# Performance work log

Hardware: AMD Instinct MI355X
Metric: run time of the kernel (lower is better)

Reference implementation:

```python
import jax, jax.numpy as jnp
import numpy as np

VOCAB, DIM, LAYERS = 32000, 1024, 4
B, L = 8, 512


def setup_inputs() -> dict:
    key = jax.random.key(0)
    ks = jax.random.split(key, 8)
    s = 0.02
    return {
        "input_ids": jax.random.randint(ks[0], (B, L), 0, VOCAB),
        "embed_W": jax.random.normal(ks[1], (VOCAB, DIM), jnp.float32) * s,
        "h_starter": jax.random.normal(ks[2], (LAYERS, DIM), jnp.float32) * s,
        "gate_W": jax.random.normal(ks[3], (LAYERS, 2 * DIM, 2 * DIM), jnp.float32) * s,
        "gate_b": jnp.zeros((LAYERS, 2 * DIM), jnp.float32),
        "cand_W": jax.random.normal(ks[4], (LAYERS, DIM, 2 * DIM), jnp.float32) * s,
        "cand_b": jnp.zeros((LAYERS, DIM), jnp.float32),
        "out_W": jax.random.normal(ks[5], (VOCAB, DIM), jnp.float32) * s,
    }


def _gru_forward(input_ids, embed_W, h_starter, gate_W, gate_b, cand_W, cand_b, out_W):
    Bsz = input_ids.shape[0]
    x = embed_W[input_ids]                      # [B, L, D]
    h0 = jnp.broadcast_to(h_starter[:, None, :], (LAYERS, Bsz, DIM))  # [Ly, B, D]

    def step(h, x_t):
        # h: [Ly, B, D], x_t: [B, D]
        new_h = []
        xin = x_t
        for i in range(LAYERS):
            hi = h[i]
            xh = jnp.concatenate([xin, hi], axis=-1)           # [B, 2D]
            g = xh @ gate_W[i].T + gate_b[i]                   # [B, 2D]
            z, r = jnp.split(g, 2, axis=-1)
            z = jax.nn.sigmoid(z)
            r = jax.nn.sigmoid(r)
            cin = jnp.concatenate([xin, r * hi], axis=-1)      # [B, 2D]
            cand = jnp.tanh(cin @ cand_W[i].T + cand_b[i])     # [B, D]
            hn = z * hi + (1.0 - z) * cand
            new_h.append(hn)
            xin = hn
        return jnp.stack(new_h), xin

    _, ys = jax.lax.scan(step, h0, jnp.swapaxes(x, 0, 1))      # ys: [L, B, D]
    ys = jnp.swapaxes(ys, 0, 1)                                # [B, L, D]
    logits = jnp.einsum('bld,vd->blv', ys, out_W)              # [B, L, V]
    return logits


def reference(input_ids, embed_W, h_starter, gate_W, gate_b, cand_W, cand_b, out_W):
    return _gru_forward(input_ids, embed_W, h_starter, gate_W, gate_b, cand_W, cand_b, out_W)
```

## Files before the change

### kernel.cpp

```cpp
#include <hip/hip_runtime.h>
#include <hip/hip_bf16.h>

#define VOCAB  32000
#define DIM    1024
#define NLAYER 4
#define NB     8
#define SEQ    512

#define NGROUP       4
#define GBLKS        64
#define SCAN_BLOCKS  (NGROUP * GBLKS)
#define SCAN_THREADS 512
#define ROWH         2056

typedef __attribute__((ext_vector_type(8))) short          bf16x8;
typedef __attribute__((ext_vector_type(4))) float          f32x4;
typedef __attribute__((ext_vector_type(8))) unsigned short u16x8;
typedef __attribute__((ext_vector_type(8))) _Float16       h8f;

__device__ __forceinline__ u16x8 cvt8_bf16(const float* p) {
    float4 f0 = *(const float4*)p;
    float4 f1 = *(const float4*)(p + 4);
    union { __hip_bfloat16 h[8]; u16x8 v; } u;
    u.h[0] = __float2bfloat16(f0.x); u.h[1] = __float2bfloat16(f0.y);
    u.h[2] = __float2bfloat16(f0.z); u.h[3] = __float2bfloat16(f0.w);
    u.h[4] = __float2bfloat16(f1.x); u.h[5] = __float2bfloat16(f1.y);
    u.h[6] = __float2bfloat16(f1.z); u.h[7] = __float2bfloat16(f1.w);
    return u.v;
}

__device__ __forceinline__ h8f pack8(f32x4 a, f32x4 b) {
    h8f o;
    o[0] = (_Float16)a[0]; o[1] = (_Float16)a[1];
    o[2] = (_Float16)a[2]; o[3] = (_Float16)a[3];
    o[4] = (_Float16)b[0]; o[5] = (_Float16)b[1];
    o[6] = (_Float16)b[2]; o[7] = (_Float16)b[3];
    return o;
}

__device__ __forceinline__ void ld4v(f32x4& d, const float* p) {
    asm volatile("global_load_dwordx4 %0, %1, off sc0 sc1"
                 : "=&v"(d) : "v"(p));
}
__device__ __forceinline__ void st1v(float* p, float v) {
    asm volatile("global_store_dword %0, %1, off sc0 sc1"
                 :: "v"(p), "v"(v) : "memory");
}
__device__ __forceinline__ void vmwait0() {
    asm volatile("s_waitcnt vmcnt(0)" ::: "memory");
}

__global__ void bar_init_kernel(unsigned* __restrict__ bar) {
    bar[threadIdx.x]        = 0u;
    bar[threadIdx.x + 1024] = 0u;
    bar[threadIdx.x + 2048] = 0u;
    bar[threadIdx.x + 3072] = 0u;
}

__device__ __forceinline__ void slot_bar(unsigned* __restrict__ slots, int bkg,
                                         unsigned seq, bool& dead) {
    __syncthreads();
    const int tid = threadIdx.x;
    if (tid == 0)
        __hip_atomic_store(&slots[bkg * 8], seq, __ATOMIC_RELAXED,
                           __HIP_MEMORY_SCOPE_AGENT);
    if (tid < 64 && !dead) {
        unsigned guard = 0;
        for (;;) {
            unsigned v = __hip_atomic_load(&slots[tid * 8], __ATOMIC_RELAXED,
                                           __HIP_MEMORY_SCOPE_AGENT);
            if (__all((int)(v >= seq))) break;
            __builtin_amdgcn_s_sleep(1);
            if (++guard > (1u << 16)) { dead = true; break; }
        }
    }
    __syncthreads();
}

__global__ void __launch_bounds__(SCAN_THREADS)
__attribute__((amdgpu_waves_per_eu(2, 2)))
gru_scan(
    const int*   __restrict__ ids,
    const float* __restrict__ embW,
    const float* __restrict__ hstart,
    const float* __restrict__ gW,
    const float* __restrict__ gB,
    const float* __restrict__ cW,
    const float* __restrict__ cB,
    float* __restrict__ hbuf,
    float* __restrict__ rbuf,
    float* __restrict__ ysf,
    unsigned* __restrict__ bar)
{
    __shared__ _Float16 act[NB][ROWH];
    __shared__ float pz[4][4][64];
    __shared__ float pr[4][4][64];
    __shared__ float pc[2][4][64];
    __shared__ float pcb[2][4][64];

    const int tid   = threadIdx.x;
    const int lane  = tid & 63;
    const int wv    = tid >> 6;
    const int l15   = lane & 15;
    const int lgq   = lane >> 4;
    const int bcol  = l15 & 7;
    const int g     = blockIdx.x >> 6;
    const int bkg   = blockIdx.x & (GBLKS-1);
    const int jbase = bkg * 16;
    const int jrow  = jbase + l15;

    h8f Wa[16], Wb[16];
    if (wv < 4) {
        const int kb = wv * 512;
        const float* wzp = gW + ((size_t)g * 2048 + jrow) * 2048;
        const float* wrp = gW + ((size_t)g * 2048 + 1024 + jrow) * 2048;
        #pragma unroll
        for (int kc = 0; kc < 16; ++kc) {
            const int k0 = kb + kc * 32 + lgq * 8;
            Wa[kc] = pack8(*(const f32x4*)(wzp + k0), *(const f32x4*)(wzp + k0 + 4));
            Wb[kc] = pack8(*(const f32x4*)(wrp + k0), *(const f32x4*)(wrp + k0 + 4));
        }
        #pragma unroll
        for (int kc = 0; kc < 16; ++kc) {
            asm volatile("" : "+v"(Wa[kc]));
            asm volatile("" : "+v"(Wb[kc]));
        }
    } else if (wv < 6) {
        const int kb = (wv - 4) * 512;
        const float* wcp = cW + ((size_t)g * 1024 + jrow) * 2048;
        #pragma unroll
        for (int kc = 0; kc < 16; ++kc) {
            const int k0 = kb + kc * 32 + lgq * 8;
            Wa[kc] = pack8(*(const f32x4*)(wcp + k0), *(const f32x4*)(wcp + k0 + 4));
            Wb[kc] = pack8(*(const f32x4*)(wcp + 1024 + k0), *(const f32x4*)(wcp + 1024 + k0 + 4));
        }
        #pragma unroll
        for (int kc = 0; kc < 16; ++kc) {
            asm volatile("" : "+v"(Wa[kc]));
            asm volatile("" : "+v"(Wb[kc]));
        }
    }

    float bz4[4], br4[4], cb4[4], hold[4], zreg[4];
    if (wv == 6) {
        #pragma unroll
        for (int r = 0; r < 4; ++r) {
            const int j = jbase + lgq * 4 + r;
            bz4[r]  = gB[g * 2048 + j];
            cb4[r]  = cB[g * 1024 + j];
            hold[r] = hstart[g * 1024 + j];
        }
    }
    if (wv == 7) {
        #pragma unroll
        for (int r = 0; r < 4; ++r)
            br4[r] = gB[g * 2048 + 1024 + jbase + lgq * 4 + r];
    }

    bool dead = false;
    unsigned* slots1g = bar + g * 512;
    unsigned* slots2g = bar + 2048 + g * 512;
    unsigned* s2prev  = (g > 0)          ? bar + 2048 + (g - 1) * 512 : nullptr;
    unsigned* s1next  = (g < NGROUP - 1) ? bar + (g + 1) * 512        : nullptr;
    float* rbufg = rbuf + (size_t)g * NB * DIM;

    if (tid < 128) {
        int e = bkg * 128 + tid;
        st1v(&hbuf[((size_t)3 * NLAYER + g) * NB * DIM + e],
             hstart[g * DIM + (e & (DIM - 1))]);
    }
    slot_bar(slots2g, bkg, 1u, dead);

    for (int t = 0; t < SEQ; ++t) {
        const int so = (t + 3) & 3;
        const int sw = t & 3;
        const float* hsrc = hbuf + ((size_t)so * NLAYER + g) * NB * DIM;
        float*       hdst = hbuf + ((size_t)sw * NLAYER + g) * NB * DIM;

        {
            const unsigned need_a = (g > 0) ? (unsigned)(t + 2) : 0u;
            const unsigned need_b = (g < NGROUP - 1 && t >= 4) ? (unsigned)(t - 3) : 0u;
            if (tid < 64 && !dead && (need_a | need_b)) {
                unsigned guard = 0;
                for (;;) {
                    bool ok = true;
                    if (need_a)
                        ok &= (__hip_atomic_load(&s2prev[tid * 8], __ATOMIC_RELAXED,
                                                 __HIP_MEMORY_SCOPE_AGENT) >= need_a);
                    if (need_b)
                        ok &= (__hip_atomic_load(&s1next[tid * 8], __ATOMIC_RELAXED,
                                                 __HIP_MEMORY_SCOPE_AGENT) >= need_b);
                    if (__all((int)ok)) break;
                    __builtin_amdgcn_s_sleep(1);
                    if (++guard > (1u << 16)) { dead = true; break; }
                }
            }
            __syncthreads();
        }

        {
            const int ub = tid & 127;
            const int b0 = tid >> 7;
            f32x4 xv0, xv1, xv2, xv3, hv0, hv1, hv2, hv3;
            if (g == 0) {
                const float* s0 = embW + (size_t)ids[b0 * SEQ + t] * DIM + ub * 8;
                const float* s1 = embW + (size_t)ids[(b0 + 4) * SEQ + t] * DIM + ub * 8;
                xv0 = *(const f32x4*)s0; xv1 = *(const f32x4*)(s0 + 4);
                xv2 = *(const f32x4*)s1; xv3 = *(const f32x4*)(s1 + 4);
            } else {
                const float* src = hbuf + ((size_t)sw * NLAYER + (g - 1)) * NB * DIM;
                ld4v(xv0, src + b0 * DIM + ub * 8);
                ld4v(xv1, src + b0 * DIM + ub * 8 + 4);
                ld4v(xv2, src + (b0 + 4) * DIM + ub * 8);
                ld4v(xv3, src + (b0 + 4) * DIM + ub * 8 + 4);
            }
            ld4v(hv0, hsrc + b0 * DIM + ub * 8);
            ld4v(hv1, hsrc + b0 * DIM + ub * 8 + 4);
            ld4v(hv2, hsrc + (b0 + 4) * DIM + ub * 8);
            ld4v(hv3, hsrc + (b0 + 4) * DIM + ub * 8 + 4);
            vmwait0();
            asm volatile("" : "+v"(xv0), "+v"(xv1), "+v"(xv2), "+v"(xv3),
                             "+v"(hv0), "+v"(hv1), "+v"(hv2), "+v"(hv3));
            *(h8f*)&act[b0][ub * 8]            = pack8(xv0, xv1);
            *(h8f*)&act[b0 + 4][ub * 8]        = pack8(xv2, xv3);
            *(h8f*)&act[b0][1024 + ub * 8]     = pack8(hv0, hv1);
            *(h8f*)&act[b0 + 4][1024 + ub * 8] = pack8(hv2, hv3);
        }
        __syncthreads();

        if (wv < 6) {
            const int kb2 = (wv < 4) ? wv * 512 : (wv - 4) * 512;
            f32x4 accA = {0.f, 0.f, 0.f, 0.f};
            f32x4 accB = {0.f, 0.f, 0.f, 0.f};
            #pragma unroll
            for (int kc = 0; kc < 16; ++kc) {
                const h8f bf = *(const h8f*)&act[bcol][kb2 + kc * 32 + lgq * 8];
                accA = __builtin_amdgcn_mfma_f32_16x16x32_f16(Wa[kc], bf, accA, 0, 0, 0);
                if (wv < 4)
                    accB = __builtin_amdgcn_mfma_f32_16x16x32_f16(Wb[kc], bf, accB, 0, 0, 0);
            }
            if (wv < 4) {
                #pragma unroll
                for (int r = 0; r < 4; ++r) {
                    pz[wv][r][lane] = accA[r];
                    pr[wv][r][lane] = accB[r];
                }
            } else {
                #pragma unroll
                for (int r = 0; r < 4; ++r) pc[wv - 4][r][lane] = accA[r];
            }
        }
        __syncthreads();

        if (wv == 6) {
            #pragma unroll
            for (int r = 0; r < 4; ++r) {
                const float s = pz[0][r][lane] + pz[1][r][lane]
                              + pz[2][r][lane] + pz[3][r][lane] + bz4[r];
                zreg[r] = 1.f / (1.f + expf(-s));
            }
        }
        if (wv == 7) {
            #pragma unroll
            for (int r = 0; r < 4; ++r) {
                const float s = pr[0][r][lane] + pr[1][r][lane]
                              + pr[2][r][lane] + pr[3][r][lane] + br4[r];
                const float rg = 1.f / (1.f + expf(-s));
                if (l15 < 8)
                    st1v(rbufg + bcol * DIM + jbase + lgq * 4 + r, rg);
            }
        }
        slot_bar(slots1g, bkg, (unsigned)(t + 1), dead);

        {
            const int ub = tid & 127;
            const int b0 = tid >> 7;
            f32x4 rv0, rv1, rv2, rv3;
            ld4v(rv0, rbufg + b0 * DIM + ub * 8);
            ld4v(rv1, rbufg + b0 * DIM + ub * 8 + 4);
            ld4v(rv2, rbufg + (b0 + 4) * DIM + ub * 8);
            ld4v(rv3, rbufg + (b0 + 4) * DIM + ub * 8 + 4);
            h8f hh0 = *(const h8f*)&act[b0][1024 + ub * 8];
            h8f hh1 = *(const h8f*)&act[b0 + 4][1024 + ub * 8];
            vmwait0();
            asm volatile("" : "+v"(rv0), "+v"(rv1), "+v"(rv2), "+v"(rv3));
            h8f o0, o1;
            #pragma unroll
            for (int i = 0; i < 4; ++i) {
                o0[i]     = (_Float16)((float)hh0[i]     * rv0[i]);
                o0[i + 4] = (_Float16)((float)hh0[i + 4] * rv1[i]);
                o1[i]     = (_Float16)((float)hh1[i]     * rv2[i]);
                o1[i + 4] = (_Float16)((float)hh1[i + 4] * rv3[i]);
            }
            *(h8f*)&act[b0][ub * 8]     = o0;
            *(h8f*)&act[b0 + 4][ub * 8] = o1;
        }
        __syncthreads();

        if (wv == 4 || wv == 5) {
            const int kb2 = (wv - 4) * 512;
            f32x4 acc = {0.f, 0.f, 0.f, 0.f};
            #pragma unroll
            for (int kc = 0; kc < 16; ++kc) {
                const h8f bf = *(const h8f*)&act[bcol][kb2 + kc * 32 + lgq * 8];
                acc = __builtin_amdgcn_mfma_f32_16x16x32_f16(Wb[kc], bf, acc, 0, 0, 0);
            }
            #pragma unroll
            for (int r = 0; r < 4; ++r) pcb[wv - 4][r][lane] = acc[r];
        }
        __syncthreads();

        if (wv == 6) {
            #pragma unroll
            for (int r = 0; r < 4; ++r) {
                const float cand = tanhf(pc[0][r][lane] + pc[1][r][lane]
                                         + pcb[0][r][lane] + pcb[1][r][lane] + cb4[r]);
                const float hn = zreg[r] * hold[r] + (1.f - zreg[r]) * cand;
                hold[r] = hn;
                if (l15 < 8) {
                    const int j = jbase + lgq * 4 + r;
                    st1v(hdst + bcol * DIM + j, hn);
                    if (g == NGROUP - 1)
                        ysf[((size_t)bcol * SEQ + t) * DIM + j] = hn;
                }
            }
        }
        slot_bar(slots2g, bkg, (unsigned)(t + 2), dead);
    }

    if (dead && tid == 0)
        ysf[blockIdx.x] = 1.0e8f;
}

#define BM 128
#define BN 128
#define BK 64

__global__ void __launch_bounds__(256) out_gemm(
    const float* __restrict__ A,
    const float* __restrict__ B,
    float* __restrict__ C)
{
    __shared__ __hip_bfloat16 At[BM][BK + 8];
    __shared__ __hip_bfloat16 Bt[BN][BK + 8];

    const int tid  = threadIdx.x;
    const int lane = tid & 63;
    const int wv   = tid >> 6;
    const int wm   = wv >> 1, wn = wv & 1;
    const int m0   = blockIdx.y * BM;
    const int n0   = blockIdx.x * BN;

    f32x4 acc[4][4];
    #pragma unroll
    for (int i = 0; i < 4; ++i)
        #pragma unroll
        for (int jj = 0; jj < 4; ++jj)
            acc[i][jj] = (f32x4){0.f, 0.f, 0.f, 0.f};

    const int srow = tid >> 3;
    const int scol = (tid & 7) * 8;
    const int l15  = lane & 15;
    const int l4   = lane >> 4;

    for (int kt = 0; kt < DIM / BK; ++kt) {
        const int k0 = kt * BK;
        #pragma unroll
        for (int rnd = 0; rnd < 4; ++rnd) {
            const int row = rnd * 32 + srow;
            *(u16x8*)&At[row][scol] =
                cvt8_bf16(&A[(size_t)(m0 + row) * DIM + k0 + scol]);
            *(u16x8*)&Bt[row][scol] =
                cvt8_bf16(&B[(size_t)(n0 + row) * DIM + k0 + scol]);
        }
        __syncthreads();
        #pragma unroll
        for (int ks = 0; ks < 2; ++ks) {
            bf16x8 av[4], bv[4];
            #pragma unroll
            for (int i = 0; i < 4; ++i) {
                av[i] = *(const bf16x8*)&At[wm * 64 + i * 16 + l15][ks * 32 + l4 * 8];
                bv[i] = *(const bf16x8*)&Bt[wn * 64 + i * 16 + l15][ks * 32 + l4 * 8];
            }
            #pragma unroll
            for (int i = 0; i < 4; ++i)
                #pragma unroll
                for (int jj = 0; jj < 4; ++jj)
                    acc[i][jj] = __builtin_amdgcn_mfma_f32_16x16x32_bf16(
                        av[i], bv[jj], acc[i][jj], 0, 0, 0);
        }
        __syncthreads();
    }

    const int rq = l4 * 4;
    #pragma unroll
    for (int i = 0; i < 4; ++i) {
        const int rbase = m0 + wm * 64 + i * 16 + rq;
        #pragma unroll
        for (int jj = 0; jj < 4; ++jj) {
            const int col = n0 + wn * 64 + jj * 16 + l15;
            #pragma unroll
            for (int r2 = 0; r2 < 4; ++r2)
                C[(size_t)(rbase + r2) * VOCAB + col] = acc[i][jj][r2];
        }
    }
}

extern "C" void kernel_launch(void* const* d_in, const int* in_sizes, int n_in,
                              void* d_out, int out_size, void* d_ws, size_t ws_size,
                              hipStream_t stream)
{
    (void)in_sizes; (void)n_in; (void)out_size; (void)ws_size;
    const int*   ids  = (const int*)  d_in[0];
    const float* embW = (const float*)d_in[1];
    const float* hst  = (const float*)d_in[2];
    const float* gW   = (const float*)d_in[3];
    const float* gB   = (const float*)d_in[4];
    const float* cW   = (const float*)d_in[5];
    const float* cB   = (const float*)d_in[6];
    const float* outW = (const float*)d_in[7];
    float* logits = (float*)d_out;

    char* ws = (char*)d_ws;
    unsigned* bar  = (unsigned*)ws;
    float*    rbuf = (float*)(ws + 16384);
    float*    hbuf = (float*)(ws + 16384 + 131072);
    float*    ysf  = (float*)(ws + 16384 + 131072 + 524288);

    bar_init_kernel<<<dim3(1), dim3(1024), 0, stream>>>(bar);

    gru_scan<<<dim3(SCAN_BLOCKS), dim3(SCAN_THREADS), 0, stream>>>(
        ids, embW, hst, gW, gB, cW, cB, hbuf, rbuf, ysf, bar);

    out_gemm<<<dim3(VOCAB / BN, (NB * SEQ) / BM), dim3(256), 0, stream>>>(ysf, outW, logits);
}
```

Baseline: 4.163 ms.

## Stream fp16 state directly into MFMA operands, drop LDS staging and syncs

The per-step exchange buffers for hidden state and r*h become fp16, and r*h is computed by the gate wave before publishing, so the candidate waves load MFMA B-operands straight from global memory instead of staging everything through a shared activation array. Waits on the previous and next group are moved into only the waves that need them, and two block-wide syncs per step are removed. The final-layer output is written as bf16 so the output GEMM skips its fp32-to-bf16 conversion. In exchange the state exchange loses precision and each wave issues more scattered small global loads.

Result: slower. 6.747 ms (+62.1%).

```diff
diff --git a/kernel.cpp b/kernel.cpp
--- a/kernel.cpp
+++ b/kernel.cpp
@@ -11,12 +11,14 @@
 #define GBLKS        64
 #define SCAN_BLOCKS  (NGROUP * GBLKS)
 #define SCAN_THREADS 512
-#define ROWH         2056
 
 typedef __attribute__((ext_vector_type(8))) short          bf16x8;
 typedef __attribute__((ext_vector_type(4))) float          f32x4;
+typedef __attribute__((ext_vector_type(2))) float          f32x2;
 typedef __attribute__((ext_vector_type(8))) unsigned short u16x8;
+typedef __attribute__((ext_vector_type(4))) unsigned short u16x4;
 typedef __attribute__((ext_vector_type(8))) _Float16       h8f;
+typedef __attribute__((ext_vector_type(4))) _Float16       h4f;
 
 __device__ __forceinline__ u16x8 cvt8_bf16(const float* p) {
     float4 f0 = *(const float4*)p;
@@ -42,8 +44,12 @@
     asm volatile("global_load_dwordx4 %0, %1, off sc0 sc1"
                  : "=&v"(d) : "v"(p));
 }
-__device__ __forceinline__ void st1v(float* p, float v) {
-    asm volatile("global_store_dword %0, %1, off sc0 sc1"
+__device__ __forceinline__ void st8v(void* p, f32x2 v) {
+    asm volatile("global_store_dwordx2 %0, %1, off sc0 sc1"
+                 :: "v"(p), "v"(v) : "memory");
+}
+__device__ __forceinline__ void st2v(void* p, unsigned v) {
+    asm volatile("global_store_short %0, %1, off sc0 sc1"
                  :: "v"(p), "v"(v) : "memory");
 }
 __device__ __forceinline__ void vmwait0() {
@@ -87,16 +93,16 @@
     const float* __restrict__ gB,
     const float* __restrict__ cW,
     const float* __restrict__ cB,
-    float* __restrict__ hbuf,
-    float* __restrict__ rbuf,
-    float* __restrict__ ysf,
+    _Float16* __restrict__ hbuf16,
+    _Float16* __restrict__ rbuf16,
+    __hip_bfloat16* __restrict__ ysfb,
     unsigned* __restrict__ bar)
 {
-    __shared__ _Float16 act[NB][ROWH];
     __shared__ float pz[4][4][64];
     __shared__ float pr[4][4][64];
     __shared__ float pc[2][4][64];
     __shared__ float pcb[2][4][64];
+    __shared__ float hb[4][64];
 
     const int tid   = threadIdx.x;
     const int lane  = tid & 63;
@@ -109,30 +115,30 @@
     const int jbase = bkg * 16;
     const int jrow  = jbase + l15;
 
+    const bool xwave = (wv == 0 || wv == 1 || wv == 4 || wv == 5);
+    const int  xoff  = (wv == 1 || wv == 5) ? 512 : 0;
+    const int  hoff  = (wv == 3) ? 512 : 0;
+
     h8f Wa[16], Wb[16];
-    if (wv < 4) {
-        const int kb = wv * 512;
+    if (wv < 6) {
         const float* wzp = gW + ((size_t)g * 2048 + jrow) * 2048;
         const float* wrp = gW + ((size_t)g * 2048 + 1024 + jrow) * 2048;
+        const float* wcp = cW + ((size_t)g * 1024 + jrow) * 2048;
+        const float* baseA; const float* baseB; int koA, koB;
+        switch (wv) {
+          case 0:  baseA = wzp; koA = 0;    baseB = wrp; koB = 0;    break;
+          case 1:  baseA = wzp; koA = 512;  baseB = wrp; koB = 512;  break;
+          case 2:  baseA = wzp; koA = 1024; baseB = wrp; koB = 1024; break;
+          case 3:  baseA = wzp; koA = 1536; baseB = wrp; koB = 1536; break;
+          case 4:  baseA = wcp; koA = 0;    baseB = wcp; koB = 1024; break;
+          default: baseA = wcp; koA = 512;  baseB = wcp; koB = 1536; break;
+        }
         #pragma unroll
         for (int kc = 0; kc < 16; ++kc) {
-            const int k0 = kb + kc * 32 + lgq * 8;
-            Wa[kc] = pack8(*(const f32x4*)(wzp + k0), *(const f32x4*)(wzp + k0 + 4));
-            Wb[kc] = pack8(*(const f32x4*)(wrp + k0), *(const f32x4*)(wrp + k0 + 4));
-        }
-        #pragma unroll
-        for (int kc = 0; kc < 16; ++kc) {
-            asm volatile("" : "+v"(Wa[kc]));
-            asm volatile("" : "+v"(Wb[kc]));
-        }
-    } else if (wv < 6) {
-        const int kb = (wv - 4) * 512;
-        const float* wcp = cW + ((size_t)g * 1024 + jrow) * 2048;
-        #pragma unroll
-        for (int kc = 0; kc < 16; ++kc) {
-            const int k0 = kb + kc * 32 + lgq * 8;
-            Wa[kc] = pack8(*(const f32x4*)(wcp + k0), *(const f32x4*)(wcp + k0 + 4));
-            Wb[kc] = pack8(*(const f32x4*)(wcp + 1024 + k0), *(const f32x4*)(wcp + 1024 + k0 + 4));
+            const int ka = koA + kc * 32 + lgq * 8;
+            const int kb = koB + kc * 32 + lgq * 8;
+            Wa[kc] = pack8(*(const f32x4*)(baseA + ka), *(const f32x4*)(baseA + ka + 4));
+            Wb[kc] = pack8(*(const f32x4*)(baseB + kb), *(const f32x4*)(baseB + kb + 4));
         }
         #pragma unroll
         for (int kc = 0; kc < 16; ++kc) {
@@ -149,6 +155,7 @@
             bz4[r]  = gB[g * 2048 + j];
             cb4[r]  = cB[g * 1024 + j];
             hold[r] = hstart[g * 1024 + j];
+            hb[r][lane] = hold[r];
         }
     }
     if (wv == 7) {
@@ -162,82 +169,94 @@
     unsigned* slots2g = bar + 2048 + g * 512;
     unsigned* s2prev  = (g > 0)          ? bar + 2048 + (g - 1) * 512 : nullptr;
     unsigned* s1next  = (g < NGROUP - 1) ? bar + (g + 1) * 512        : nullptr;
-    float* rbufg = rbuf + (size_t)g * NB * DIM;
+    _Float16* rbufg16 = rbuf16 + (size_t)g * NB * DIM;
 
     if (tid < 128) {
         int e = bkg * 128 + tid;
-        st1v(&hbuf[((size_t)3 * NLAYER + g) * NB * DIM + e],
-             hstart[g * DIM + (e & (DIM - 1))]);
+        union { _Float16 h; unsigned short u; } cv;
+        cv.h = (_Float16)hstart[g * DIM + (e & (DIM - 1))];
+        st2v(&hbuf16[((size_t)3 * NLAYER + g) * NB * DIM + e], (unsigned)cv.u);
     }
     slot_bar(slots2g, bkg, 1u, dead);
 
     for (int t = 0; t < SEQ; ++t) {
         const int so = (t + 3) & 3;
         const int sw = t & 3;
-        const float* hsrc = hbuf + ((size_t)so * NLAYER + g) * NB * DIM;
-        float*       hdst = hbuf + ((size_t)sw * NLAYER + g) * NB * DIM;
-
-        {
-            const unsigned need_a = (g > 0) ? (unsigned)(t + 2) : 0u;
-            const unsigned need_b = (g < NGROUP - 1 && t >= 4) ? (unsigned)(t - 3) : 0u;
-            if (tid < 64 && !dead && (need_a | need_b)) {
-                unsigned guard = 0;
-                for (;;) {
-                    bool ok = true;
-                    if (need_a)
-                        ok &= (__hip_atomic_load(&s2prev[tid * 8], __ATOMIC_RELAXED,
-                                                 __HIP_MEMORY_SCOPE_AGENT) >= need_a);
-                    if (need_b)
-                        ok &= (__hip_atomic_load(&s1next[tid * 8], __ATOMIC_RELAXED,
-                                                 __HIP_MEMORY_SCOPE_AGENT) >= need_b);
-                    if (__all((int)ok)) break;
-                    __builtin_amdgcn_s_sleep(1);
-                    if (++guard > (1u << 16)) { dead = true; break; }
-                }
-            }
-            __syncthreads();
-        }
-
-        {
-            const int ub = tid & 127;
-            const int b0 = tid >> 7;
-            f32x4 xv0, xv1, xv2, xv3, hv0, hv1, hv2, hv3;
-            if (g == 0) {
-                const float* s0 = embW + (size_t)ids[b0 * SEQ + t] * DIM + ub * 8;
-                const float* s1 = embW + (size_t)ids[(b0 + 4) * SEQ + t] * DIM + ub * 8;
-                xv0 = *(const f32x4*)s0; xv1 = *(const f32x4*)(s0 + 4);
-                xv2 = *(const f32x4*)s1; xv3 = *(const f32x4*)(s1 + 4);
-            } else {
-                const float* src = hbuf + ((size_t)sw * NLAYER + (g - 1)) * NB * DIM;
-                ld4v(xv0, src + b0 * DIM + ub * 8);
-                ld4v(xv1, src + b0 * DIM + ub * 8 + 4);
-                ld4v(xv2, src + (b0 + 4) * DIM + ub * 8);
-                ld4v(xv3, src + (b0 + 4) * DIM + ub * 8 + 4);
-            }
-            ld4v(hv0, hsrc + b0 * DIM + ub * 8);
-            ld4v(hv1, hsrc + b0 * DIM + ub * 8 + 4);
-            ld4v(hv2, hsrc + (b0 + 4) * DIM + ub * 8);
-            ld4v(hv3, hsrc + (b0 + 4) * DIM + ub * 8 + 4);
-            vmwait0();
-            asm volatile("" : "+v"(xv0), "+v"(xv1), "+v"(xv2), "+v"(xv3),
-                             "+v"(hv0), "+v"(hv1), "+v"(hv2), "+v"(hv3));
-            *(h8f*)&act[b0][ub * 8]            = pack8(xv0, xv1);
-            *(h8f*)&act[b0 + 4][ub * 8]        = pack8(xv2, xv3);
-            *(h8f*)&act[b0][1024 + ub * 8]     = pack8(hv0, hv1);
-            *(h8f*)&act[b0 + 4][1024 + ub * 8] = pack8(hv2, hv3);
-        }
-        __syncthreads();
+        const _Float16* hsrc16 = hbuf16 + ((size_t)so * NLAYER + g) * NB * DIM;
+        _Float16*       hdst16 = hbuf16 + ((size_t)sw * NLAYER + g) * NB * DIM;
+        const _Float16* xprev16 = hbuf16 + ((size_t)sw * NLAYER + (g > 0 ? g - 1 : 0)) * NB * DIM;
+
+        if (g > 0 && xwave && !dead) {
+            const unsigned need = (unsigned)(t + 2);
+            unsigned guard = 0;
+            for (;;) {
+                unsigned v = __hip_atomic_load(&s2prev[lane * 8], __ATOMIC_RELAXED,
+                                               __HIP_MEMORY_SCOPE_AGENT);
+                if (__all((int)(v >= need))) break;
+                __builtin_amdgcn_s_sleep(1);
+                if (++guard > (1u << 16)) { dead = true; break; }
+            }
+        }
+        if (wv == 6 && g < NGROUP - 1 && t >= 4 && !dead) {
+            const unsigned need = (unsigned)(t - 3);
+            unsigned guard = 0;
+            for (;;) {
+                unsigned v = __hip_atomic_load(&s1next[lane * 8], __ATOMIC_RELAXED,
+                                               __HIP_MEMORY_SCOPE_AGENT);
+                if (__all((int)(v >= need))) break;
+                __builtin_amdgcn_s_sleep(1);
+                if (++guard > (1u << 16)) { dead = true; break; }
+            }
+        }
 
         if (wv < 6) {
-            const int kb2 = (wv < 4) ? wv * 512 : (wv - 4) * 512;
             f32x4 accA = {0.f, 0.f, 0.f, 0.f};
             f32x4 accB = {0.f, 0.f, 0.f, 0.f};
-            #pragma unroll
-            for (int kc = 0; kc < 16; ++kc) {
-                const h8f bf = *(const h8f*)&act[bcol][kb2 + kc * 32 + lgq * 8];
-                accA = __builtin_amdgcn_mfma_f32_16x16x32_f16(Wa[kc], bf, accA, 0, 0, 0);
-                if (wv < 4)
-                    accB = __builtin_amdgcn_mfma_f32_16x16x32_f16(Wb[kc], bf, accB, 0, 0, 0);
+            if (g == 0 && xwave) {
+                const int erow = ids[bcol * SEQ + t];
+                const float* ep = embW + (size_t)erow * DIM + xoff;
+                #pragma unroll
+                for (int c = 0; c < 2; ++c) {
+                    f32x4 c0[8], c1[8];
+                    #pragma unroll
+                    for (int k8 = 0; k8 < 8; ++k8) {
+                        const float* p = ep + (c * 8 + k8) * 32 + lgq * 8;
+                        ld4v(c0[k8], p);
+                        ld4v(c1[k8], p + 4);
+                    }
+                    vmwait0();
+                    #pragma unroll
+                    for (int k8 = 0; k8 < 8; ++k8) {
+                        asm volatile("" : "+v"(c0[k8]));
+                        asm volatile("" : "+v"(c1[k8]));
+                    }
+                    #pragma unroll
+                    for (int k8 = 0; k8 < 8; ++k8) {
+                        const int kc = c * 8 + k8;
+                        const h8f bf = pack8(c0[k8], c1[k8]);
+                        accA = __builtin_amdgcn_mfma_f32_16x16x32_f16(Wa[kc], bf, accA, 0, 0, 0);
+                        if (wv < 4)
+                            accB = __builtin_amdgcn_mfma_f32_16x16x32_f16(Wb[kc], bf, accB, 0, 0, 0);
+                    }
+                }
+            } else {
+                const _Float16* bsrc = xwave ? (xprev16 + (size_t)bcol * DIM + xoff)
+                                             : (hsrc16 + (size_t)bcol * DIM + hoff);
+                f32x4 braw[16];
+                #pragma unroll
+                for (int kc = 0; kc < 16; ++kc)
+                    ld4v(braw[kc], (const float*)(bsrc + kc * 32 + lgq * 8));
+                vmwait0();
+                #pragma unroll
+                for (int kc = 0; kc < 16; ++kc)
+                    asm volatile("" : "+v"(braw[kc]));
+                #pragma unroll
+                for (int kc = 0; kc < 16; ++kc) {
+                    const h8f bf = __builtin_bit_cast(h8f, braw[kc]);
+                    accA = __builtin_amdgcn_mfma_f32_16x16x32_f16(Wa[kc], bf, accA, 0, 0, 0);
+                    if (wv < 4)
+                        accB = __builtin_amdgcn_mfma_f32_16x16x32_f16(Wb[kc], bf, accB, 0, 0, 0);
+                }
             }
             if (wv < 4) {
                 #pragma unroll
@@ -261,75 +280,70 @@
             }
         }
         if (wv == 7) {
+            h4f rh4;
             #pragma unroll
             for (int r = 0; r < 4; ++r) {
                 const float s = pr[0][r][lane] + pr[1][r][lane]
                               + pr[2][r][lane] + pr[3][r][lane] + br4[r];
                 const float rg = 1.f / (1.f + expf(-s));
-                if (l15 < 8)
-                    st1v(rbufg + bcol * DIM + jbase + lgq * 4 + r, rg);
-            }
+                rh4[r] = (_Float16)(rg * hb[r][lane]);
+            }
+            if (l15 < 8)
+                st8v(rbufg16 + (size_t)bcol * DIM + jbase + lgq * 4,
+                     __builtin_bit_cast(f32x2, rh4));
         }
         slot_bar(slots1g, bkg, (unsigned)(t + 1), dead);
 
-        {
-            const int ub = tid & 127;
-            const int b0 = tid >> 7;
-            f32x4 rv0, rv1, rv2, rv3;
-            ld4v(rv0, rbufg + b0 * DIM + ub * 8);
-            ld4v(rv1, rbufg + b0 * DIM + ub * 8 + 4);
-            ld4v(rv2, rbufg + (b0 + 4) * DIM + ub * 8);
-            ld4v(rv3, rbufg + (b0 + 4) * DIM + ub * 8 + 4);
-            h8f hh0 = *(const h8f*)&act[b0][1024 + ub * 8];
-            h8f hh1 = *(const h8f*)&act[b0 + 4][1024 + ub * 8];
+        if (wv == 4 || wv == 5) {
+            const _Float16* rsrc = rbufg16 + (size_t)bcol * DIM + ((wv == 5) ? 512 : 0);
+            f32x4 rraw[16];
+            #pragma unroll
+            for (int kc = 0; kc < 16; ++kc)
+                ld4v(rraw[kc], (const float*)(rsrc + kc * 32 + lgq * 8));
             vmwait0();
-            asm volatile("" : "+v"(rv0), "+v"(rv1), "+v"(rv2), "+v"(rv3));
-            h8f o0, o1;
-            #pragma unroll
-            for (int i = 0; i < 4; ++i) {
-                o0[i]     = (_Float16)((float)hh0[i]     * rv0[i]);
-                o0[i + 4] = (_Float16)((float)hh0[i + 4] * rv1[i]);
-                o1[i]     = (_Float16)((float)hh1[i]     * rv2[i]);
-                o1[i + 4] = (_Float16)((float)hh1[i + 4] * rv3[i]);
-            }
-            *(h8f*)&act[b0][ub * 8]     = o0;
-            *(h8f*)&act[b0 + 4][ub * 8] = o1;
+            #pragma unroll
+            for (int kc = 0; kc < 16; ++kc)
+                asm volatile("" : "+v"(rraw[kc]));
+            f32x4 acc = {0.f, 0.f, 0.f, 0.f};
+            #pragma unroll
+            for (int kc = 0; kc < 16; ++kc)
+                acc = __builtin_amdgcn_mfma_f32_16x16x32_f16(
+                    Wb[kc], __builtin_bit_cast(h8f, rraw[kc]), acc, 0, 0, 0);
+            #pragma unroll
+            for (int r = 0; r < 4; ++r) pcb[wv - 4][r][lane] = acc[r];
         }
         __syncthreads();
 
-        if (wv == 4 || wv == 5) {
-            const int kb2 = (wv - 4) * 512;
-            f32x4 acc = {0.f, 0.f, 0.f, 0.f};
-            #pragma unroll
-            for (int kc = 0; kc < 16; ++kc) {
-                const h8f bf = *(const h8f*)&act[bcol][kb2 + kc * 32 + lgq * 8];
-                acc = __builtin_amdgcn_mfma_f32_16x16x32_f16(Wb[kc], bf, acc, 0, 0, 0);
-            }
-            #pragma unroll
-            for (int r = 0; r < 4; ++r) pcb[wv - 4][r][lane] = acc[r];
-        }
-        __syncthreads();
-
         if (wv == 6) {
+            h4f hp; u16x4 yp;
             #pragma unroll
             for (int r = 0; r < 4; ++r) {
                 const float cand = tanhf(pc[0][r][lane] + pc[1][r][lane]
                                          + pcb[0][r][lane] + pcb[1][r][lane] + cb4[r]);
                 const float hn = zreg[r] * hold[r] + (1.f - zreg[r]) * cand;
                 hold[r] = hn;
-                if (l15 < 8) {
-                    const int j = jbase + lgq * 4 + r;
-                    st1v(hdst + bcol * DIM + j, hn);
-                    if (g == NGROUP - 1)
-                        ysf[((size_t)bcol * SEQ + t) * DIM + j] = hn;
-                }
+                hb[r][lane] = hn;
+                hp[r] = (_Float16)hn;
+                union { __hip_bfloat16 b; unsigned short u; } cv;
+                cv.b = __float2bfloat16(hn);
+                yp[r] = cv.u;
+            }
+            if (l15 < 8) {
+                st8v(hdst16 + (size_t)bcol * DIM + jbase + lgq * 4,
+                     __builtin_bit_cast(f32x2, hp));
+                if (g == NGROUP - 1)
+                    *(f32x2*)(ysfb + ((size_t)bcol * SEQ + t) * DIM + jbase + lgq * 4) =
+                        __builtin_bit_cast(f32x2, yp);
             }
         }
         slot_bar(slots2g, bkg, (unsigned)(t + 2), dead);
     }
 
-    if (dead && tid == 0)
-        ysf[blockIdx.x] = 1.0e8f;
+    if (dead && tid == 0) {
+        union { __hip_bfloat16 b; unsigned short u; } cv;
+        cv.b = __float2bfloat16(1.0e8f);
+        ((unsigned short*)ysfb)[blockIdx.x] = cv.u;
+    }
 }
 
 #define BM 128
@@ -337,7 +351,7 @@
 #define BK 64
 
 __global__ void __launch_bounds__(256) out_gemm(
-    const float* __restrict__ A,
+    const __hip_bfloat16* __restrict__ A,
     const float* __restrict__ B,
     float* __restrict__ C)
 {
@@ -369,7 +383,7 @@
         for (int rnd = 0; rnd < 4; ++rnd) {
             const int row = rnd * 32 + srow;
             *(u16x8*)&At[row][scol] =
-                cvt8_bf16(&A[(size_t)(m0 + row) * DIM + k0 + scol]);
+                *(const u16x8*)&A[(size_t)(m0 + row) * DIM + k0 + scol];
             *(u16x8*)&Bt[row][scol] =
                 cvt8_bf16(&B[(size_t)(n0 + row) * DIM + k0 + scol]);
         }
@@ -422,15 +436,15 @@
     float* logits = (float*)d_out;
 
     char* ws = (char*)d_ws;
-    unsigned* bar  = (unsigned*)ws;
-    float*    rbuf = (float*)(ws + 16384);
-    float*    hbuf = (float*)(ws + 16384 + 131072);
-    float*    ysf  = (float*)(ws + 16384 + 131072 + 524288);
+    unsigned*       bar     = (unsigned*)ws;
+    _Float16*       rbuf16  = (_Float16*)(ws + 16384);
+    _Float16*       hbuf16  = (_Float16*)(ws + 16384 + 65536);
+    __hip_bfloat16* ysfb    = (__hip_bfloat16*)(ws + 16384 + 65536 + 262144);
 
     bar_init_kernel<<<dim3(1), dim3(1024), 0, stream>>>(bar);
 
     gru_scan<<<dim3(SCAN_BLOCKS), dim3(SCAN_THREADS), 0, stream>>>(
-        ids, embW, hst, gW, gB, cW, cB, hbuf, rbuf, ysf, bar);
-
-    out_gemm<<<dim3(VOCAB / BN, (NB * SEQ) / BM), dim3(256), 0, stream>>>(ysf, outW, logits);
-}
+        ids, embW, hst, gW, gB, cW, cB, hbuf16, rbuf16, ysfb, bar);
+
+    out_gemm<<<dim3(VOCAB / BN, (NB * SEQ) / BM), dim3(256), 0, stream>>>(ysfb, outW, logits);
+}
```
